# Kernel optimization log

Hardware: AMD Instinct MI355X
Metric: run time of the kernel (lower is better)

## Reference

```python
import jax, jax.numpy as jnp
import numpy as np

NT, NS, NH, NG, NR = 730, 2000, 16, 32, 15


def _lin_params(key, fan_in, fan_out):
    k1, k2 = jax.random.split(key)
    s = 1.0 / np.sqrt(fan_in)
    W = jax.random.uniform(k1, (fan_out, fan_in), minval=-s, maxval=s, dtype=jnp.float32)
    b = jax.random.uniform(k2, (fan_out,), minval=-s, maxval=s, dtype=jnp.float32)
    return W, b


def setup_inputs() -> dict:
    key = jax.random.key(0)
    ks = jax.random.split(key, 10)
    x = jax.random.normal(ks[0], (NT, NS, 6), dtype=jnp.float32)
    xc = jax.random.normal(ks[1], (NS, NG), dtype=jnp.float32)
    fc_W1, fc_b1 = _lin_params(ks[2], NG, 256)
    fc_W2, fc_b2 = _lin_params(ks[3], 256, NH * 10)
    fcR_W1, fcR_b1 = _lin_params(ks[4], NG, 256)
    fcR_W2, fcR_b2 = _lin_params(ks[5], 256, NH * NR)
    fcT1_W1, fcT1_b1 = _lin_params(ks[6], 1 + NG, 256)
    fcT1_W2, fcT1_b2 = _lin_params(ks[7], 256, NH * 2)
    fcT2_W1, fcT2_b1 = _lin_params(ks[8], 3 + NG, 256)
    fcT2_W2, fcT2_b2 = _lin_params(ks[9], 256, NH + 1)
    return dict(x=x, xc=xc,
                fc_W1=fc_W1, fc_b1=fc_b1, fc_W2=fc_W2, fc_b2=fc_b2,
                fcR_W1=fcR_W1, fcR_b1=fcR_b1, fcR_W2=fcR_W2, fcR_b2=fcR_b2,
                fcT1_W1=fcT1_W1, fcT1_b1=fcT1_b1, fcT1_W2=fcT1_W2, fcT1_b2=fcT1_b2,
                fcT2_W1=fcT2_W1, fcT2_b1=fcT2_b1, fcT2_W2=fcT2_W2, fcT2_b2=fcT2_b2)


def _mlp(z, W1, b1, W2, b2):
    # Linear -> Tanh -> Dropout(eval: identity) -> Linear
    h = jnp.tanh(z @ W1.T + b1)
    return h @ W2.T + b2


def _conv_ts(x, r):
    # causal per-(basin, bucket) temporal routing convolution
    # x: [nt, ns, nh], r: [ns, nh*nr] (relu'd routing weights)
    nt, ns, nh = x.shape
    nr = r.shape[-1] // nh
    xr = jnp.transpose(x, (1, 2, 0)).reshape(1, ns * nh, nt)   # [1, ns*nh, nt]
    k = r.reshape(ns * nh, 1, nr)
    y = jax.lax.conv_general_dilated(xr, k, (1,), [(nr - 1, 0)],
                                     feature_group_count=ns * nh)
    return jnp.transpose(y.reshape(ns, nh, nt), (2, 0, 1))     # [nt, ns, nh]


def _hsig(z):
    # F.hardsigmoid
    return jnp.clip(z / 6.0 + 0.5, 0.0, 1.0)


def _forward(x, xc, fc_W1, fc_b1, fc_W2, fc_b2, fcR_W1, fcR_b1, fcR_W2, fcR_b2,
             fcT1_W1, fcT1_b1, fcT1_W2, fcT1_b2, fcT2_W1, fcT2_b1, fcT2_W2, fcT2_b2):
    P, E, T1, T2, R, LAI = [x[:, :, i] for i in range(6)]
    nt, ns = P.shape
    nh = NH

    # snow/rain partition vp; masked positions get safe ratio to avoid nan grads
    mask = (T1 >= 0) | (T2 <= 0)
    denom = T2 - T1
    ratio = jnp.clip((T1 + T2) / jnp.where(denom == 0, 1.0, denom), -1.0, 1.0)
    ratio = jnp.where(mask, 0.0, ratio)
    vp = 1.0 - jnp.arccos(ratio) / 3.1415
    vp = jnp.where(T1 >= 0, 1.0, vp)
    vp = jnp.where(T2 <= 0, 0.0, vp)

    w = _mlp(xc, fc_W1, fc_b1, fc_W2, fc_b2)        # [ns, nh*10]
    wR = _mlp(xc, fcR_W1, fcR_b1, fcR_W2, fcR_b2)   # [ns, nh*nr]
    xc_t = jnp.broadcast_to(xc, (nt, ns, xc.shape[-1]))
    xcT1 = jnp.concatenate([LAI[:, :, None], xc_t], axis=-1)
    xcT2 = jnp.concatenate([R[:, :, None], T1[:, :, None], T2[:, :, None], xc_t], axis=-1)
    v1 = _mlp(xcT1, fcT1_W1, fcT1_b1, fcT1_W2, fcT1_b2)  # [nt, ns, nh*2]
    v2 = _mlp(xcT2, fcT2_W1, fcT2_b1, fcT2_W2, fcT2_b2)  # [nt, ns, nh+1]

    k1 = jax.nn.sigmoid(w[:, nh:2 * nh])
    k2 = jax.nn.sigmoid(w[:, 2 * nh:3 * nh])
    k23 = jax.nn.sigmoid(w[:, 3 * nh:4 * nh])
    k3 = jax.nn.sigmoid(w[:, 4 * nh:5 * nh]) / 10
    gl = jnp.exp(w[:, 5 * nh:6 * nh]) * 2
    ga = jax.nn.softmax(w[:, 6 * nh:7 * nh], axis=1)
    qb = jax.nn.relu(w[:, 7 * nh:8 * nh])
    ge1 = jax.nn.relu(w[:, 8 * nh:9 * nh])
    ge2 = jax.nn.relu(w[:, 9 * nh:10 * nh])

    vi = _hsig(v1[:, :, :nh])
    vk = _hsig(v1[:, :, nh:2 * nh])
    vm = jnp.exp(v2[:, :, :nh] * 2)

    Ps = P * (1 - vp)                     # [nt, ns]
    Pl = P * vp
    Pl1 = Pl[:, :, None] * (1 - vi)       # [nt, ns, nh]
    Pl2 = Pl[:, :, None] * vi
    Ev1 = E[:, :, None] * ge1
    Ev2 = E[:, :, None] * ge2

    def step(carry, inp):
        S0, Sv, S2, S3 = carry
        Ps_k, Pl1_k, Pl2_k, Ev1_k, Ev2_k, vk_k, vm_k = inp
        H0 = S0 + Ps_k[:, None]
        qSm = jnp.minimum(H0, vm_k)
        Hv = jax.nn.relu(Sv + Pl1_k - Ev1_k)
        qv = Sv * vk_k
        H2 = jax.nn.relu(S2 + qSm + qv - Ev2_k + Pl2_k)
        x1 = H2 - gl
        pos = x1 > 0
        Q1 = jnp.where(pos, jnp.power(jnp.where(pos, x1, 1.0), k1), 0.0)
        q2 = jnp.minimum(H2, gl) * k2
        Q2 = q2 * (1 - k23)
        H3 = S3 + q2 * k23
        Q3 = H3 * k3 + qb
        return (H0 - qSm, Hv - qv, H2 - Q1 - q2, H3 - Q3), (Q1, Q2, Q3)

    z = jnp.zeros((ns, nh), dtype=x.dtype)
    _, (Q1T, Q2T, Q3T) = jax.lax.scan(step, (z, z, z, z),
                                      (Ps, Pl1, Pl2, Ev1, Ev2, vk, vm))

    r = jax.nn.relu(wR)
    Q1R = _conv_ts(Q1T, r)
    Q2R = _conv_ts(Q2T, r)
    Q3R = _conv_ts(Q3T, r)
    return jnp.sum((Q1R + Q2R + Q3R) * ga, axis=2)   # [nt, ns]


def reference(x, xc, fc_W1, fc_b1, fc_W2, fc_b2, fcR_W1, fcR_b1, fcR_W2, fcR_b2,
              fcT1_W1, fcT1_b1, fcT1_W2, fcT1_b2, fcT2_W1, fcT2_b1, fcT2_W2, fcT2_b2):
    return _forward(x, xc, fc_W1, fc_b1, fc_W2, fc_b2, fcR_W1, fcR_b1, fcR_W2, fcR_b2,
                    fcT1_W1, fcT1_b1, fcT1_W2, fcT1_b2, fcT2_W1, fcT2_b1, fcT2_W2, fcT2_b2)
```

## Files before the change

### kernel.cpp

```cpp
#include <hip/hip_runtime.h>
#include <math.h>

#define NT 730
#define NS 2000
#define NH 16
#define NG 32
#define NR 15
#define HID 256
#define NSNH 32000

#define SC 2.885390081777927f
#define INV6 0.16666666666666666f

typedef _Float16 f16x8 __attribute__((ext_vector_type(8)));
typedef __fp16 fp16v2 __attribute__((ext_vector_type(2)));
typedef float f32x4 __attribute__((ext_vector_type(4)));

__device__ __forceinline__ float tanh_pre(float y) {
    float e = __builtin_amdgcn_exp2f(y);
    float r = __builtin_amdgcn_rcpf(e + 1.f);
    return fmaf(-2.f, r, 1.f);
}
__device__ __forceinline__ float fast_tanh(float x) { return tanh_pre(x * SC); }
__device__ __forceinline__ float sigmoidf_(float x) { return 1.f / (1.f + __expf(-x)); }

__device__ __forceinline__ float rcp_pre(float y) {
    float e = __builtin_amdgcn_exp2f(y);
    return __builtin_amdgcn_rcpf(e + 1.f);
}
__device__ __forceinline__ f16x8 rcp8(float4 lo, float4 hi) {
    union { fp16v2 h[4]; f16x8 v; } u;
    u.h[0] = __builtin_amdgcn_cvt_pkrtz(rcp_pre(lo.x), rcp_pre(lo.y));
    u.h[1] = __builtin_amdgcn_cvt_pkrtz(rcp_pre(lo.z), rcp_pre(lo.w));
    u.h[2] = __builtin_amdgcn_cvt_pkrtz(rcp_pre(hi.x), rcp_pre(hi.y));
    u.h[3] = __builtin_amdgcn_cvt_pkrtz(rcp_pre(hi.z), rcp_pre(hi.w));
    return u.v;
}

__global__ __launch_bounds__(256) void k_basin(
    const float* __restrict__ XC,
    const float* __restrict__ fcW1, const float* __restrict__ fcb1,
    const float* __restrict__ fcW2, const float* __restrict__ fcb2,
    const float* __restrict__ fRW1, const float* __restrict__ fRb1,
    const float* __restrict__ fRW2, const float* __restrict__ fRb2,
    const float* __restrict__ T1W1, const float* __restrict__ T1b1,
    const float* __restrict__ T2W1, const float* __restrict__ T2b1,
    const float* __restrict__ T1W2, const float* __restrict__ T1b2,
    const float* __restrict__ T2W2, const float* __restrict__ T2b2,
    float* __restrict__ P8, float* __restrict__ RKGA,
    float2* __restrict__ BASE12,
    float4* __restrict__ CC4, _Float16* __restrict__ W2H,
    float* __restrict__ BIAS48)
{
    const int tid = threadIdx.x;

    if (blockIdx.x == NS / 4) {
        int k = tid;
        CC4[k] = make_float4(SC * T1W1[k * (1 + NG)],
                             SC * T2W1[k * (3 + NG)],
                             SC * T2W1[k * (3 + NG) + 1],
                             SC * T2W1[k * (3 + NG) + 2]);
        for (int c = 0; c < 48; ++c) {
            float w = (c < 32) ? (INV6 * T1W2[c * HID + k]) : (SC * T2W2[(c - 32) * HID + k]);
            W2H[c * HID + k] = (_Float16)(-2.f * w);
        }
        if (k < 48) {
            float s = 0.f;
            if (k < 32) {
                for (int i = 0; i < HID; ++i)
                    s += -0.5f * (float)(_Float16)(-2.f * INV6 * T1W2[k * HID + i]);
                BIAS48[k] = fmaf(T1b2[k], INV6, 0.5f) + s;
            } else {
                for (int i = 0; i < HID; ++i)
                    s += -0.5f * (float)(_Float16)(-2.f * SC * T2W2[(k - 32) * HID + i]);
                BIAS48[k] = SC * T2b2[k - 32] + s;
            }
        }
        return;
    }

    const int s0 = blockIdx.x * 4;
    __shared__ float xcs[4][NG];
    __shared__ float h[4][HID], hR[4][HID];
    __shared__ float wbuf[4][10 * NH], wRbuf[4][NH * NR];
    __shared__ float gav[4][NH];

    if (tid < 128) xcs[tid >> 5][tid & 31] = XC[(s0 + (tid >> 5)) * NG + (tid & 31)];
    __syncthreads();

    {
        float ab0 = fcb1[tid], ab1 = ab0, ab2 = ab0, ab3 = ab0;
        float rb0 = fRb1[tid], rb1 = rb0, rb2 = rb0, rb3 = rb0;
        const float4* w4  = (const float4*)(fcW1 + tid * NG);
        const float4* wR4 = (const float4*)(fRW1 + tid * NG);
#pragma unroll
        for (int g = 0; g < NG / 4; ++g) {
            float4 wv = w4[g], rv = wR4[g];
            float4 x0 = *(const float4*)&xcs[0][g * 4];
            float4 x1 = *(const float4*)&xcs[1][g * 4];
            float4 x2 = *(const float4*)&xcs[2][g * 4];
            float4 x3 = *(const float4*)&xcs[3][g * 4];
            ab0 += x0.x*wv.x + x0.y*wv.y + x0.z*wv.z + x0.w*wv.w;
            ab1 += x1.x*wv.x + x1.y*wv.y + x1.z*wv.z + x1.w*wv.w;
            ab2 += x2.x*wv.x + x2.y*wv.y + x2.z*wv.z + x2.w*wv.w;
            ab3 += x3.x*wv.x + x3.y*wv.y + x3.z*wv.z + x3.w*wv.w;
            rb0 += x0.x*rv.x + x0.y*rv.y + x0.z*rv.z + x0.w*rv.w;
            rb1 += x1.x*rv.x + x1.y*rv.y + x1.z*rv.z + x1.w*rv.w;
            rb2 += x2.x*rv.x + x2.y*rv.y + x2.z*rv.z + x2.w*rv.w;
            rb3 += x3.x*rv.x + x3.y*rv.y + x3.z*rv.z + x3.w*rv.w;
        }
        h[0][tid] = fast_tanh(ab0); h[1][tid] = fast_tanh(ab1);
        h[2][tid] = fast_tanh(ab2); h[3][tid] = fast_tanh(ab3);
        hR[0][tid] = fast_tanh(rb0); hR[1][tid] = fast_tanh(rb1);
        hR[2][tid] = fast_tanh(rb2); hR[3][tid] = fast_tanh(rb3);

        float b10 = T1b1[tid], b11 = b10, b12 = b10, b13 = b10;
        float b20 = T2b1[tid], b21 = b20, b22 = b20, b23 = b20;
        const float* w1 = T1W1 + tid * (1 + NG) + 1;
        const float* w2 = T2W1 + tid * (3 + NG) + 3;
#pragma unroll 8
        for (int g = 0; g < NG; ++g) {
            float w1g = w1[g], w2g = w2[g];
            float x0 = xcs[0][g], x1 = xcs[1][g], x2 = xcs[2][g], x3 = xcs[3][g];
            b10 = fmaf(x0, w1g, b10); b11 = fmaf(x1, w1g, b11);
            b12 = fmaf(x2, w1g, b12); b13 = fmaf(x3, w1g, b13);
            b20 = fmaf(x0, w2g, b20); b21 = fmaf(x1, w2g, b21);
            b22 = fmaf(x2, w2g, b22); b23 = fmaf(x3, w2g, b23);
        }
        BASE12[(size_t)(s0 + 0) * HID + tid] = make_float2(SC * b10, SC * b20);
        BASE12[(size_t)(s0 + 1) * HID + tid] = make_float2(SC * b11, SC * b21);
        BASE12[(size_t)(s0 + 2) * HID + tid] = make_float2(SC * b12, SC * b22);
        BASE12[(size_t)(s0 + 3) * HID + tid] = make_float2(SC * b13, SC * b23);
    }
    __syncthreads();

    if (tid < 10 * NH) {
        float a0 = fcb2[tid], a1 = a0, a2 = a0, a3 = a0;
        const float4* w4 = (const float4*)(fcW2 + tid * HID);
        for (int k = 0; k < HID / 4; ++k) {
            float4 wv = w4[k];
            float4 h0 = *(const float4*)&h[0][k * 4];
            float4 h1 = *(const float4*)&h[1][k * 4];
            float4 h2 = *(const float4*)&h[2][k * 4];
            float4 h3 = *(const float4*)&h[3][k * 4];
            a0 += h0.x*wv.x + h0.y*wv.y + h0.z*wv.z + h0.w*wv.w;
            a1 += h1.x*wv.x + h1.y*wv.y + h1.z*wv.z + h1.w*wv.w;
            a2 += h2.x*wv.x + h2.y*wv.y + h2.z*wv.z + h2.w*wv.w;
            a3 += h3.x*wv.x + h3.y*wv.y + h3.z*wv.z + h3.w*wv.w;
        }
        wbuf[0][tid] = a0; wbuf[1][tid] = a1; wbuf[2][tid] = a2; wbuf[3][tid] = a3;
    }
    if (tid < NH * NR) {
        float a0 = fRb2[tid], a1 = a0, a2 = a0, a3 = a0;
        const float4* w4 = (const float4*)(fRW2 + tid * HID);
        for (int k = 0; k < HID / 4; ++k) {
            float4 wv = w4[k];
            float4 h0 = *(const float4*)&hR[0][k * 4];
            float4 h1 = *(const float4*)&hR[1][k * 4];
            float4 h2 = *(const float4*)&hR[2][k * 4];
            float4 h3 = *(const float4*)&hR[3][k * 4];
            a0 += h0.x*wv.x + h0.y*wv.y + h0.z*wv.z + h0.w*wv.w;
            a1 += h1.x*wv.x + h1.y*wv.y + h1.z*wv.z + h1.w*wv.w;
            a2 += h2.x*wv.x + h2.y*wv.y + h2.z*wv.z + h2.w*wv.w;
            a3 += h3.x*wv.x + h3.y*wv.y + h3.z*wv.z + h3.w*wv.w;
        }
        wRbuf[0][tid] = a0; wRbuf[1][tid] = a1; wRbuf[2][tid] = a2; wRbuf[3][tid] = a3;
    }
    __syncthreads();

    if (tid < 64) {
        int b = tid >> 4, hh = tid & 15;
        const float* wb = wbuf[b];
        float mx = -1e30f;
        for (int i = 0; i < NH; ++i) mx = fmaxf(mx, wb[6 * NH + i]);
        float sum = 0.f;
        for (int i = 0; i < NH; ++i) sum += expf(wb[6 * NH + i] - mx);
        gav[b][hh] = expf(wb[6 * NH + hh] - mx) / sum;

        float* p = P8 + (size_t)((s0 + b) * NH + hh) * 8;
        p[0] = sigmoidf_(wb[1 * NH + hh]);
        p[1] = sigmoidf_(wb[2 * NH + hh]);
        p[2] = sigmoidf_(wb[3 * NH + hh]);
        p[3] = sigmoidf_(wb[4 * NH + hh]) * 0.1f;
        p[4] = expf(wb[5 * NH + hh]) * 2.f;
        p[5] = fmaxf(wb[7 * NH + hh], 0.f);
        p[6] = fmaxf(wb[8 * NH + hh], 0.f);
        p[7] = fmaxf(wb[9 * NH + hh], 0.f);
    }
    __syncthreads();

    for (int it = tid; it < 4 * NH * NR; it += 256) {
        int b = it / (NH * NR), r = it % (NH * NR);
        int hh = r / NR, j = r % NR;
        RKGA[(size_t)((s0 + b) * NH + hh) * 16 + (NR - 1 - j)] =
            gav[b][hh] * fmaxf(wRbuf[b][hh * NR + j], 0.f);
    }
}

__device__ __forceinline__ void store_pse(float4* __restrict__ PSE, long m, float2 pe, float2 t12) {
    float P = pe.x, E = pe.y, T1 = t12.x, T2 = t12.y;
    float den = T2 - T1;
    float ratio = (T1 + T2) / ((den == 0.f) ? 1.f : den);
    ratio = fminf(fmaxf(ratio, -1.f), 1.f);
    if ((T1 >= 0.f) || (T2 <= 0.f)) ratio = 0.f;
    float vp = 1.f - acosf(ratio) * (1.f / 3.1415f);
    if (T1 >= 0.f) vp = 1.f;
    if (T2 <= 0.f) vp = 0.f;
    PSE[m] = make_float4(P * (1.f - vp), P * vp, E, 0.f);
}

__global__ __launch_bounds__(128) void k_mlp(
    const float* __restrict__ X,
    const float2* __restrict__ BASE12, const float4* __restrict__ CC4,
    const _Float16* __restrict__ W2H, const float* __restrict__ BIAS48,
    uint2* __restrict__ VMK, float4* __restrict__ PSE)
{
    const int lane = threadIdx.x & 63;
    const int wave = threadIdx.x >> 6;
    const int quad = lane >> 4, ml = lane & 15;
    const int s0 = blockIdx.x * 16;
    const int t0 = (blockIdx.y * 2 + wave) * 4;
    const int srow = s0 + ml;

    const int tc0 = (t0 < NT) ? t0 : (NT - 1);
    const int tc1 = (t0 + 1 < NT) ? t0 + 1 : (NT - 1);
    const int tc2 = (t0 + 2 < NT) ? t0 + 2 : (NT - 1);
    const int tc3 = (t0 + 3 < NT) ? t0 + 3 : (NT - 1);

    const float* xr0 = X + ((long)tc0 * NS + srow) * 6;
    const float* xr1 = X + ((long)tc1 * NS + srow) * 6;
    const float* xr2 = X + ((long)tc2 * NS + srow) * 6;
    const float* xr3 = X + ((long)tc3 * NS + srow) * 6;
    float2 tt0 = *(const float2*)(xr0 + 2), rl0 = *(const float2*)(xr0 + 4);
    float2 tt1 = *(const float2*)(xr1 + 2), rl1 = *(const float2*)(xr1 + 4);
    float2 tt2 = *(const float2*)(xr2 + 2), rl2 = *(const float2*)(xr2 + 4);
    float2 tt3 = *(const float2*)(xr3 + 2), rl3 = *(const float2*)(xr3 + 4);

    const float bvi = BIAS48[ml];
    const float bvk = BIAS48[NH + ml];
    const float bvm = BIAS48[2 * NH + ml];
    f32x4 ac0_0 = {bvi, bvi, bvi, bvi}, ac0_1 = ac0_0, ac0_2 = ac0_0, ac0_3 = ac0_0;
    f32x4 ac1_0 = {bvk, bvk, bvk, bvk}, ac1_1 = ac1_0, ac1_2 = ac1_0, ac1_3 = ac1_0;
    f32x4 ac2_0 = {bvm, bvm, bvm, bvm}, ac2_1 = ac2_0, ac2_2 = ac2_0, ac2_3 = ac2_0;

    const float2* b12p = BASE12 + (size_t)srow * HID;
    const _Float16* wvi = W2H + (size_t)ml * HID;
    const _Float16* wvk = W2H + (size_t)(NH + ml) * HID;
    const _Float16* wvm = W2H + (size_t)(2 * NH + ml) * HID;

#pragma unroll 2
    for (int ks = 0; ks < 8; ++ks) {
        const int kb = ks * 32 + quad * 8;
        float4 cc0 = CC4[kb], cc1 = CC4[kb + 1], cc2 = CC4[kb + 2], cc3 = CC4[kb + 3];
        float4 cc4 = CC4[kb + 4], cc5 = CC4[kb + 5], cc6 = CC4[kb + 6], cc7 = CC4[kb + 7];
        float4 bA = *(const float4*)(b12p + kb);
        float4 bB = *(const float4*)(b12p + kb + 2);
        float4 bC = *(const float4*)(b12p + kb + 4);
        float4 bD = *(const float4*)(b12p + kb + 6);
        f16x8 Bvi = *(const f16x8*)(wvi + kb);
        f16x8 Bvk = *(const f16x8*)(wvk + kb);
        f16x8 Bvm = *(const f16x8*)(wvm + kb);

#define ARG2(CC, B2, TT, RL) fmaf(TT.y, CC.w, fmaf(TT.x, CC.z, fmaf(RL.x, CC.y, B2)))
#define DO_TILE(RL, TT, AC0, AC1, AC2) { \
        float4 a1lo = make_float4(fmaf(RL.y, cc0.x, bA.x), fmaf(RL.y, cc1.x, bA.z), \
                                  fmaf(RL.y, cc2.x, bB.x), fmaf(RL.y, cc3.x, bB.z)); \
        float4 a1hi = make_float4(fmaf(RL.y, cc4.x, bC.x), fmaf(RL.y, cc5.x, bC.z), \
                                  fmaf(RL.y, cc6.x, bD.x), fmaf(RL.y, cc7.x, bD.z)); \
        f16x8 Af1 = rcp8(a1lo, a1hi); \
        float4 a2lo = make_float4(ARG2(cc0, bA.y, TT, RL), ARG2(cc1, bA.w, TT, RL), \
                                  ARG2(cc2, bB.y, TT, RL), ARG2(cc3, bB.w, TT, RL)); \
        float4 a2hi = make_float4(ARG2(cc4, bC.y, TT, RL), ARG2(cc5, bC.w, TT, RL), \
                                  ARG2(cc6, bD.y, TT, RL), ARG2(cc7, bD.w, TT, RL)); \
        f16x8 Af2 = rcp8(a2lo, a2hi); \
        AC0 = __builtin_amdgcn_mfma_f32_16x16x32_f16(Af1, Bvi, AC0, 0, 0, 0); \
        AC1 = __builtin_amdgcn_mfma_f32_16x16x32_f16(Af1, Bvk, AC1, 0, 0, 0); \
        AC2 = __builtin_amdgcn_mfma_f32_16x16x32_f16(Af2, Bvm, AC2, 0, 0, 0); }

        DO_TILE(rl0, tt0, ac0_0, ac1_0, ac2_0)
        DO_TILE(rl1, tt1, ac0_1, ac1_1, ac2_1)
        DO_TILE(rl2, tt2, ac0_2, ac1_2, ac2_2)
        DO_TILE(rl3, tt3, ac0_3, ac1_3, ac2_3)
#undef DO_TILE
#undef ARG2
    }

#define EPI(TC, AC0, AC1, AC2) { \
    long rowbase = (long)TC * NS + s0 + quad * 4; \
    _Pragma("unroll") \
    for (int rg = 0; rg < 4; ++rg) { \
        float vi = fminf(fmaxf(AC0[rg], 0.f), 1.f); \
        float vk = fminf(fmaxf(AC1[rg], 0.f), 1.f); \
        float vm = __builtin_amdgcn_exp2f(AC2[rg]); \
        unsigned pk = (unsigned)(vi * 65535.f + 0.5f) | ((unsigned)(vk * 65535.f + 0.5f) << 16); \
        VMK[(rowbase + rg) * NH + ml] = make_uint2(pk, __float_as_uint(vm)); \
    } }

    EPI(tc0, ac0_0, ac1_0, ac2_0)
    EPI(tc1, ac0_1, ac1_1, ac2_1)
    EPI(tc2, ac0_2, ac1_2, ac2_2)
    EPI(tc3, ac0_3, ac1_3, ac2_3)
#undef EPI

    {
        int tq = t0 + quad; if (tq >= NT) tq = NT - 1;
        const float* xq = X + ((long)tq * NS + srow) * 6;
        float2 peq = *(const float2*)xq;
        float2 ttq = *(const float2*)(xq + 2);
        store_pse(PSE, (long)tq * NS + srow, peq, ttq);
    }
}

__global__ __launch_bounds__(64) void k_scan(
    const uint2* __restrict__ VMK, const float4* __restrict__ PSE,
    const float* __restrict__ P8, const float* __restrict__ RKGA,
    _Float16* __restrict__ YH)
{
    int lane = threadIdx.x;
    int s = blockIdx.x * 4 + (lane >> 4);
    int hh = lane & 15;
    size_t ch = (size_t)s * NH + hh;

    const float4* pp = (const float4*)(P8 + (size_t)ch * 8);
    float4 pa = pp[0], pb4 = pp[1];
    float k1 = pa.x, k2 = pa.y, k23 = pa.z, k3 = pa.w;
    float gl = pb4.x, qb = pb4.y, ge1 = pb4.z, ge2 = pb4.w;

    float rk[16];
    {
        const float4* rp = (const float4*)(RKGA + (size_t)ch * 16);
#pragma unroll
        for (int i = 0; i < 4; ++i) {
            float4 v = rp[i];
            rk[4 * i] = v.x; rk[4 * i + 1] = v.y; rk[4 * i + 2] = v.z; rk[4 * i + 3] = v.w;
        }
    }

    float S0 = 0.f, Sv = 0.f, S2 = 0.f, S3 = 0.f;
    float qr[14];
#pragma unroll
    for (int i = 0; i < 14; ++i) qr[i] = 0.f;

    uint2 vb[14]; float4 pbf[14];
#pragma unroll
    for (int i = 0; i < 14; ++i) {
        vb[i] = VMK[(size_t)i * NSNH + ch];
        pbf[i] = PSE[(size_t)i * NS + s];
    }

    int t = 0;
#define SBODY(I) { \
    uint2 v = vb[I]; float4 ps = pbf[I]; \
    int t2 = t + 14; if (t2 > NT - 1) t2 = NT - 1; \
    vb[I] = VMK[(size_t)t2 * NSNH + ch]; \
    pbf[I] = PSE[(size_t)t2 * NS + s]; \
    float vi = (float)(v.x & 0xffffu) * (1.f / 65535.f); \
    float vk = (float)(v.x >> 16) * (1.f / 65535.f); \
    float vm = __uint_as_float(v.y); \
    float Ps = ps.x, Pl = ps.y, E = ps.z; \
    float H0 = S0 + Ps; \
    float qSm = fminf(H0, vm); S0 = H0 - qSm; \
    float Hv = fmaxf(Sv + Pl * (1.f - vi) - E * ge1, 0.f); \
    float qv = Sv * vk; Sv = Hv - qv; \
    float H2 = fmaxf(S2 + qSm + qv - E * ge2 + Pl * vi, 0.f); \
    float x1 = H2 - gl; \
    float Q1 = (x1 > 0.f) ? __expf(k1 * __logf(x1)) : 0.f; \
    float q2 = fminf(H2, gl) * k2; \
    float Q2 = q2 * (1.f - k23); \
    float H3 = S3 + q2 * k23; \
    float Q3 = H3 * k3 + qb; \
    S2 = H2 - Q1 - q2; S3 = H3 - Q3; \
    float qt = Q1 + Q2 + Q3; \
    float y = qt * rk[0]; \
    _Pragma("unroll") for (int d = 1; d <= 14; ++d) y += qr[((I) + 14 - d) % 14] * rk[d]; \
    qr[I] = qt; \
    YH[(size_t)t * NSNH + ch] = (_Float16)y; \
    ++t; }

    for (int tb = 0; tb < 52; ++tb) {
        SBODY(0) SBODY(1) SBODY(2) SBODY(3) SBODY(4) SBODY(5) SBODY(6)
        SBODY(7) SBODY(8) SBODY(9) SBODY(10) SBODY(11) SBODY(12) SBODY(13)
    }
    SBODY(0) SBODY(1)
#undef SBODY
}

__global__ __launch_bounds__(256) void k_reduce(
    const _Float16* __restrict__ YH, float* __restrict__ OUT)
{
    long m = (long)blockIdx.x * 256 + threadIdx.x;
    if (m >= (long)NT * NS) return;
    int t = (int)(m / NS), s = (int)(m % NS);
    const _Float16* q = YH + (size_t)t * NSNH + (size_t)s * NH;
    f16x8 a = *(const f16x8*)q;
    f16x8 b = *(const f16x8*)(q + 8);
    float acc = 0.f;
#pragma unroll
    for (int i = 0; i < 8; ++i) acc += (float)a[i];
#pragma unroll
    for (int i = 0; i < 8; ++i) acc += (float)b[i];
    OUT[m] = acc;
}

extern "C" void kernel_launch(void* const* d_in, const int* in_sizes, int n_in,
                              void* d_out, int out_size, void* d_ws, size_t ws_size,
                              hipStream_t stream)
{
    const float* X    = (const float*)d_in[0];
    const float* XC   = (const float*)d_in[1];
    const float* fcW1 = (const float*)d_in[2];
    const float* fcb1 = (const float*)d_in[3];
    const float* fcW2 = (const float*)d_in[4];
    const float* fcb2 = (const float*)d_in[5];
    const float* fRW1 = (const float*)d_in[6];
    const float* fRb1 = (const float*)d_in[7];
    const float* fRW2 = (const float*)d_in[8];
    const float* fRb2 = (const float*)d_in[9];
    const float* T1W1 = (const float*)d_in[10];
    const float* T1b1 = (const float*)d_in[11];
    const float* T1W2 = (const float*)d_in[12];
    const float* T1b2 = (const float*)d_in[13];
    const float* T2W1 = (const float*)d_in[14];
    const float* T2b1 = (const float*)d_in[15];
    const float* T2W2 = (const float*)d_in[16];
    const float* T2b2 = (const float*)d_in[17];
    float* OUT = (float*)d_out;

    char* w = (char*)d_ws;
    uint2* VMK     = (uint2*)w;     w += (size_t)NT * NSNH * 8;
    float4* PSE    = (float4*)w;    w += (size_t)NT * NS * 16;
    _Float16* YH   = (_Float16*)w;  w += (size_t)NT * NSNH * 2;
    float2* BASE12 = (float2*)w;    w += (size_t)NS * HID * 8;
    float* P8      = (float*)w;     w += (size_t)NS * NH * 8 * 4;
    float* RKGA    = (float*)w;     w += (size_t)NS * NH * 16 * 4;
    _Float16* W2H  = (_Float16*)w;  w += 48 * HID * 2;
    float4* CC4    = (float4*)w;    w += HID * 16;
    float* BIAS48  = (float*)w;     w += 64 * 4;
    (void)ws_size; (void)in_sizes; (void)n_in; (void)out_size;

    k_basin<<<dim3(NS / 4 + 1), dim3(256), 0, stream>>>(
        XC, fcW1, fcb1, fcW2, fcb2, fRW1, fRb1, fRW2, fRb2,
        T1W1, T1b1, T2W1, T2b1, T1W2, T1b2, T2W2, T2b2,
        P8, RKGA, BASE12, CC4, W2H, BIAS48);
    k_mlp<<<dim3(125, 92), dim3(128), 0, stream>>>(
        X, BASE12, CC4, W2H, BIAS48, VMK, PSE);
    k_scan<<<dim3(NS / 4), dim3(64), 0, stream>>>(VMK, PSE, P8, RKGA, YH);
    k_reduce<<<dim3((unsigned)(((long)NT * NS + 255) / 256)), dim3(256), 0, stream>>>(YH, OUT);
}
```

Measured before the change: 508.4 us.

## Move routing convolution out of serial scan into separate parallel conv kernel

The 15-tap causal routing convolution is removed from the sequential per-channel scan loop, which now only emits the summed runoff qt as fp16. A new per-basin kernel stages a time window of qt in shared memory and computes the convolution plus the head reduction in parallel over time, replacing the old reduce kernel. The aim is to shorten the latency-bound serial scan and drop its 14-entry register history. The Q1 power is also switched to raw exp2/log builtins. The trade-off is that the conv kernel re-reads qt with strided 2-byte loads and stores the output with a stride of NS across time, and qt is rounded to fp16 before the convolution rather than after.

```diff
diff --git a/kernel.cpp b/kernel.cpp
--- a/kernel.cpp
+++ b/kernel.cpp
@@ -313,8 +313,7 @@
 
 __global__ __launch_bounds__(64) void k_scan(
     const uint2* __restrict__ VMK, const float4* __restrict__ PSE,
-    const float* __restrict__ P8, const float* __restrict__ RKGA,
-    _Float16* __restrict__ YH)
+    const float* __restrict__ P8, _Float16* __restrict__ QT)
 {
     int lane = threadIdx.x;
     int s = blockIdx.x * 4 + (lane >> 4);
@@ -326,20 +325,7 @@
     float k1 = pa.x, k2 = pa.y, k23 = pa.z, k3 = pa.w;
     float gl = pb4.x, qb = pb4.y, ge1 = pb4.z, ge2 = pb4.w;
 
-    float rk[16];
-    {
-        const float4* rp = (const float4*)(RKGA + (size_t)ch * 16);
-#pragma unroll
-        for (int i = 0; i < 4; ++i) {
-            float4 v = rp[i];
-            rk[4 * i] = v.x; rk[4 * i + 1] = v.y; rk[4 * i + 2] = v.z; rk[4 * i + 3] = v.w;
-        }
-    }
-
     float S0 = 0.f, Sv = 0.f, S2 = 0.f, S3 = 0.f;
-    float qr[14];
-#pragma unroll
-    for (int i = 0; i < 14; ++i) qr[i] = 0.f;
 
     uint2 vb[14]; float4 pbf[14];
 #pragma unroll
@@ -364,17 +350,14 @@
     float qv = Sv * vk; Sv = Hv - qv; \
     float H2 = fmaxf(S2 + qSm + qv - E * ge2 + Pl * vi, 0.f); \
     float x1 = H2 - gl; \
-    float Q1 = (x1 > 0.f) ? __expf(k1 * __logf(x1)) : 0.f; \
+    float Q1 = (x1 > 0.f) ? __builtin_amdgcn_exp2f(k1 * __builtin_amdgcn_logf(x1)) : 0.f; \
     float q2 = fminf(H2, gl) * k2; \
     float Q2 = q2 * (1.f - k23); \
     float H3 = S3 + q2 * k23; \
     float Q3 = H3 * k3 + qb; \
     S2 = H2 - Q1 - q2; S3 = H3 - Q3; \
     float qt = Q1 + Q2 + Q3; \
-    float y = qt * rk[0]; \
-    _Pragma("unroll") for (int d = 1; d <= 14; ++d) y += qr[((I) + 14 - d) % 14] * rk[d]; \
-    qr[I] = qt; \
-    YH[(size_t)t * NSNH + ch] = (_Float16)y; \
+    QT[(size_t)t * NSNH + ch] = (_Float16)qt; \
     ++t; }
 
     for (int tb = 0; tb < 52; ++tb) {
@@ -385,21 +368,44 @@
 #undef SBODY
 }
 
-__global__ __launch_bounds__(256) void k_reduce(
-    const _Float16* __restrict__ YH, float* __restrict__ OUT)
+__global__ __launch_bounds__(256) void k_conv(
+    const _Float16* __restrict__ QT, const float* __restrict__ RKGA,
+    float* __restrict__ OUT)
 {
-    long m = (long)blockIdx.x * 256 + threadIdx.x;
-    if (m >= (long)NT * NS) return;
-    int t = (int)(m / NS), s = (int)(m % NS);
-    const _Float16* q = YH + (size_t)t * NSNH + (size_t)s * NH;
-    f16x8 a = *(const f16x8*)q;
-    f16x8 b = *(const f16x8*)(q + 8);
-    float acc = 0.f;
+    const int s = blockIdx.x, tid = threadIdx.x;
+    __shared__ float qs[270][18];
+    __shared__ float rks[15][16];
+
+    if (tid < 240) {
+        int d = tid >> 4, h = tid & 15;
+        rks[d][h] = RKGA[((size_t)s * NH + h) * 16 + d];
+    }
+
+    for (int t0 = 0; t0 < NT; t0 += 256) {
+        __syncthreads();
+        for (int idx = tid; idx < 270 * 16; idx += 256) {
+            int row = idx >> 4, h = idx & 15;
+            int tg = t0 - 14 + row;
+            float v = 0.f;
+            if (tg >= 0 && tg < NT)
+                v = (float)QT[(size_t)tg * NSNH + s * NH + h];
+            qs[row][h] = v;
+        }
+        __syncthreads();
+
+        int t = t0 + tid;
+        if (t < NT) {
+            float acc = 0.f;
 #pragma unroll
-    for (int i = 0; i < 8; ++i) acc += (float)a[i];
+            for (int d = 0; d < 15; ++d) {
+                const float* qrow = qs[tid + 14 - d];
 #pragma unroll
-    for (int i = 0; i < 8; ++i) acc += (float)b[i];
-    OUT[m] = acc;
+                for (int h = 0; h < 16; ++h)
+                    acc = fmaf(qrow[h], rks[d][h], acc);
+            }
+            OUT[(size_t)t * NS + s] = acc;
+        }
+    }
 }
 
 extern "C" void kernel_launch(void* const* d_in, const int* in_sizes, int n_in,
@@ -429,7 +435,7 @@
     char* w = (char*)d_ws;
     uint2* VMK     = (uint2*)w;     w += (size_t)NT * NSNH * 8;
     float4* PSE    = (float4*)w;    w += (size_t)NT * NS * 16;
-    _Float16* YH   = (_Float16*)w;  w += (size_t)NT * NSNH * 2;
+    _Float16* QT   = (_Float16*)w;  w += (size_t)NT * NSNH * 2;
     float2* BASE12 = (float2*)w;    w += (size_t)NS * HID * 8;
     float* P8      = (float*)w;     w += (size_t)NS * NH * 8 * 4;
     float* RKGA    = (float*)w;     w += (size_t)NS * NH * 16 * 4;
@@ -444,6 +450,6 @@
         P8, RKGA, BASE12, CC4, W2H, BIAS48);
     k_mlp<<<dim3(125, 92), dim3(128), 0, stream>>>(
         X, BASE12, CC4, W2H, BIAS48, VMK, PSE);
-    k_scan<<<dim3(NS / 4), dim3(64), 0, stream>>>(VMK, PSE, P8, RKGA, YH);
-    k_reduce<<<dim3((unsigned)(((long)NT * NS + 255) / 256)), dim3(256), 0, stream>>>(YH, OUT);
-}
+    k_scan<<<dim3(NS / 4), dim3(64), 0, stream>>>(VMK, PSE, P8, QT);
+    k_conv<<<dim3(NS), dim3(256), 0, stream>>>(QT, RKGA, OUT);
+}
```

Result: slower. 655.6 us (+29.0%).
